# Kernel optimization log

Hardware: AMD Instinct MI355X
Metric: run time of the kernel (lower is better)

Reference implementation:

```python
import jax, jax.numpy as jnp
import numpy as np

B, T, S = 4, 16384, 256
V_DIM, L_DIM, E, H = 256, 768, 1024, 8
D = E // H  # head_dim = 128
SCALE = D ** -0.5
CLAMP = 50000.0


def setup_inputs() -> dict:
    key = jax.random.key(0)
    ks = jax.random.split(key, 8)
    w = lambda k, shp: jax.random.normal(k, shp, jnp.float32) * 0.03  # ~xavier scale
    return {
        'v': jax.random.normal(ks[0], (B, T, V_DIM), jnp.float32),
        'l': jax.random.normal(ks[1], (B, S, L_DIM), jnp.float32),
        'v_proj_w': w(ks[2], (V_DIM, E)), 'v_proj_b': jnp.zeros((E,), jnp.float32),
        'l_proj_w': w(ks[3], (L_DIM, E)), 'l_proj_b': jnp.zeros((E,), jnp.float32),
        'vv_w': w(ks[4], (V_DIM, E)), 'vv_b': jnp.zeros((E,), jnp.float32),
        'vl_w': w(ks[5], (L_DIM, E)), 'vl_b': jnp.zeros((E,), jnp.float32),
        'ov_w': w(ks[6], (E, V_DIM)), 'ov_b': jnp.zeros((V_DIM,), jnp.float32),
        'ol_w': w(ks[7], (E, L_DIM)), 'ol_b': jnp.zeros((L_DIM,), jnp.float32),
    }


def _heads(x):
    # [B, N, E] -> [B, H, N, D]
    b, n, _ = x.shape
    return x.reshape(b, n, H, D).transpose(0, 2, 1, 3)


def reference(v, l, v_proj_w, v_proj_b, l_proj_w, l_proj_b,
              vv_w, vv_b, vl_w, vl_b, ov_w, ov_b, ol_w, ol_b):
    b, t, _ = v.shape
    s = l.shape[1]
    q = _heads((v @ v_proj_w + v_proj_b) * SCALE)   # [B,H,T,D]
    k = _heads(l @ l_proj_w + l_proj_b)             # [B,H,S,D]
    val_v = _heads(v @ vv_w + vv_b)                 # [B,H,T,D]
    val_l = _heads(l @ vl_w + vl_b)                 # [B,H,S,D]

    attn = jnp.einsum('bhtd,bhsd->bhts', q, k)      # shared QK^T scores
    attn = jnp.clip(attn, -CLAMP, CLAMP)

    # column-direction softmax (over vision tokens) on the transpose
    attn_T = attn.transpose(0, 1, 3, 2)             # [B,H,S,T]
    attn_l = attn_T - jnp.max(attn_T, axis=-1, keepdims=True)
    attn_l = jnp.clip(attn_l, -CLAMP, CLAMP)
    attn_l = jax.nn.softmax(attn_l, axis=-1)

    # row-direction softmax (over text tokens)
    attn_v = jax.nn.softmax(attn, axis=-1)          # [B,H,T,S]

    out_v = jnp.einsum('bhts,bhsd->bhtd', attn_v, val_l)
    out_l = jnp.einsum('bhst,bhtd->bhsd', attn_l, val_v)
    out_v = out_v.transpose(0, 2, 1, 3).reshape(b, t, E)
    out_l = out_l.transpose(0, 2, 1, 3).reshape(b, s, E)
    return out_v @ ov_w + ov_b, out_l @ ol_w + ol_b
```

## Files before the change

### kernel.cpp

```cpp
#include <hip/hip_runtime.h>
#include <hip/hip_bf16.h>
#include <hip/hip_fp16.h>

#define DI __device__ __forceinline__

typedef short bf16x8 __attribute__((ext_vector_type(8)));
typedef float f32x4 __attribute__((ext_vector_type(4)));
using bf16 = __hip_bfloat16;

constexpr int Tn = 16384, Sn = 256, En = 1024;
constexpr float SCALEF = 0.08838834764831845f;
constexpr float CLAMPF = 50000.0f;

DI f32x4 mfma16(bf16x8 a, bf16x8 b, f32x4 c) {
  return __builtin_amdgcn_mfma_f32_16x16x32_bf16(a, b, c, 0, 0, 0);
}
DI unsigned short f2bu(float x) { bf16 h = __float2bfloat16(x); return *(unsigned short*)&h; }
DI unsigned int pack2(float lo, float hi) { return (unsigned)f2bu(lo) | ((unsigned)f2bu(hi) << 16); }
DI bf16x8 ldg8(const bf16* p) { return *(const bf16x8*)p; }
DI float clampf(float v) { return fminf(fmaxf(v, -CLAMPF), CLAMPF); }
DI unsigned int packh2(float a, float b) {
  __half2 h = __floats2half2_rn(a, b);
  return *(unsigned int*)&h;
}

__global__ void cast_weights(const float* __restrict__ w0, bf16* __restrict__ o0,
                             const float* __restrict__ w1, bf16* __restrict__ o1,
                             const float* __restrict__ w2, bf16* __restrict__ o2,
                             const float* __restrict__ w3, bf16* __restrict__ o3,
                             const float* __restrict__ w4, bf16* __restrict__ o4,
                             const float* __restrict__ w5, bf16* __restrict__ o5) {
  int id = blockIdx.x * 256 + threadIdx.x;
  switch (blockIdx.y) {
    case 0: if (id < 256*1024) { int k = id >> 10, n = id & 1023; o0[n*256 + k] = __float2bfloat16(w0[id]); } break;
    case 1: if (id < 256*1024) { int k = id >> 10, n = id & 1023; o1[n*256 + k] = __float2bfloat16(w1[id]); } break;
    case 2: if (id < 768*1024) { int k = id >> 10, n = id & 1023; o2[n*768 + k] = __float2bfloat16(w2[id]); } break;
    case 3: if (id < 768*1024) { int k = id >> 10, n = id & 1023; o3[n*768 + k] = __float2bfloat16(w3[id]); } break;
    case 4: if (id < 1024*256) { int k = id >> 8,  n = id & 255;  o4[n*1024 + k] = __float2bfloat16(w4[id]); } break;
    case 5: if (id < 1024*768) { int k = id / 768, n = id % 768;  o5[n*1024 + k] = __float2bfloat16(w5[id]); } break;
  }
}

template<int MODE>
__global__ __launch_bounds__(256) void gemm_kern(
    const void* __restrict__ A, const bf16* __restrict__ Bw0, const bf16* __restrict__ Bw1,
    const float* __restrict__ bias0, const float* __restrict__ bias1,
    void* __restrict__ out0, void* __restrict__ out1, int zbase)
{
  constexpr int K = (MODE == 0) ? 256 : (MODE == 1) ? 768 : 1024;
  const int z = blockIdx.z + zbase;
  const bf16* Bw = z ? Bw1 : Bw0;
  const float* bias = z ? bias1 : bias0;
  const int m0 = blockIdx.x * 128, n0 = blockIdx.y * 128;
  const int tid = threadIdx.x, lane = tid & 63;
  const int w = tid >> 6, wm = w >> 1, wn = w & 1;
  const int l15 = lane & 15, l4 = lane >> 4;

  __shared__ bf16 smem[128 * 136];
  bf16* As = smem;
  bf16* Bs = smem + 128 * 64;

  f32x4 acc[4][4];
  #pragma unroll
  for (int a = 0; a < 4; a++)
    #pragma unroll
    for (int c = 0; c < 4; c++) acc[a][c] = f32x4{0.f, 0.f, 0.f, 0.f};

  for (int k0 = 0; k0 < K; k0 += 64) {
    __syncthreads();
    #pragma unroll
    for (int it = 0; it < 4; it++) {
      int cid = it * 256 + tid;
      int row = cid >> 3, chk = cid & 7;
      uint4 va;
      if constexpr (MODE <= 1) {
        const float* ap = (const float*)A + (size_t)(m0 + row) * K + k0 + chk * 8;
        float4 f0 = *(const float4*)ap, f1 = *(const float4*)(ap + 4);
        va.x = pack2(f0.x, f0.y); va.y = pack2(f0.z, f0.w);
        va.z = pack2(f1.x, f1.y); va.w = pack2(f1.z, f1.w);
      } else {
        va = *reinterpret_cast<const uint4*>((const bf16*)A + (size_t)(m0 + row) * K + k0 + chk * 8);
      }
      *reinterpret_cast<uint4*>(As + row * 64 + ((chk ^ (row & 7)) * 8)) = va;
      uint4 vb = *reinterpret_cast<const uint4*>(Bw + (size_t)(n0 + row) * K + k0 + chk * 8);
      *reinterpret_cast<uint4*>(Bs + row * 64 + ((chk ^ (row & 7)) * 8)) = vb;
    }
    __syncthreads();
    #pragma unroll
    for (int ks = 0; ks < 2; ks++) {
      bf16x8 af[4], bfr[4];
      #pragma unroll
      for (int mf = 0; mf < 4; mf++) {
        int r = wm * 64 + mf * 16 + l15;
        af[mf] = *(const bf16x8*)(As + r * 64 + (((ks * 4 + l4) ^ (r & 7)) * 8));
      }
      #pragma unroll
      for (int nf = 0; nf < 4; nf++) {
        int r = wn * 64 + nf * 16 + l15;
        bfr[nf] = *(const bf16x8*)(Bs + r * 64 + (((ks * 4 + l4) ^ (r & 7)) * 8));
      }
      #pragma unroll
      for (int mf = 0; mf < 4; mf++)
        #pragma unroll
        for (int nf = 0; nf < 4; nf++)
          acc[mf][nf] = mfma16(af[mf], bfr[nf], acc[mf][nf]);
    }
  }
  __syncthreads();

  if constexpr (MODE <= 1) {
    #pragma unroll
    for (int nf = 0; nf < 4; nf++) {
      int nl = wn * 64 + nf * 16 + l15;
      float bv = bias[n0 + nl];
      #pragma unroll
      for (int mf = 0; mf < 4; mf++) {
        int ml = wm * 64 + mf * 16 + l4 * 4;
        #pragma unroll
        for (int i = 0; i < 4; i++) {
          float vv = acc[mf][nf][i] + bv;
          if (MODE == 0 && z == 0) vv *= SCALEF;
          smem[(ml + i) * 136 + nl] = __float2bfloat16(vv);
        }
      }
    }
    __syncthreads();
    constexpr int TT = (MODE == 0) ? Tn : Sn;
    const int h = n0 >> 7;
    const int r2 = tid >> 1, c0 = (tid & 1) * 64;
    if (z == 0) {
      int m = m0 + r2;
      int bq = (MODE == 0) ? 0 : (m >> 8);
      int t  = m & (TT - 1);
      bf16* out = (bf16*)out0;
      size_t base = ((size_t)(bq * 8 + h) * TT + t) * 128 + c0;
      #pragma unroll
      for (int j = 0; j < 32; j++) {
        unsigned int u = *(const unsigned int*)(smem + r2 * 136 + c0 + 2 * j);
        *(unsigned int*)(out + base + 2 * j) = u;
      }
    } else {
      int bq = (MODE == 0) ? 0 : (m0 >> 8);
      int t0 = m0 & (TT - 1);
      bf16* out = (bf16*)out1;
      size_t base = ((size_t)(bq * 8 + h) * 128 + r2) * TT + t0 + c0;
      #pragma unroll
      for (int j = 0; j < 32; j++) {
        unsigned short u0 = *(const unsigned short*)(smem + (c0 + 2 * j)     * 136 + r2);
        unsigned short u1 = *(const unsigned short*)(smem + (c0 + 2 * j + 1) * 136 + r2);
        *(unsigned int*)(out + base + 2 * j) = (unsigned)u0 | ((unsigned)u1 << 16);
      }
    }
  } else {
    constexpr int NOUT = (MODE == 2) ? 256 : 768;
    float* out = (float*)out0;
    #pragma unroll
    for (int nf = 0; nf < 4; nf++) {
      int n = n0 + wn * 64 + nf * 16 + l15;
      float bv = bias[n];
      #pragma unroll
      for (int mf = 0; mf < 4; mf++) {
        size_t mbase = (size_t)(m0 + wm * 64 + mf * 16 + l4 * 4) * NOUT + n;
        #pragma unroll
        for (int i = 0; i < 4; i++)
          out[mbase + (size_t)i * NOUT] = acc[mf][nf][i] + bv;
      }
    }
  }
}

template<int NCH, bool SLAB>
__global__ __launch_bounds__(512, 2) void attn_fused(
    const bf16* __restrict__ qh,
    const bf16* __restrict__ kh,
    const bf16* __restrict__ vallT,
    const bf16* __restrict__ valvT,
    bf16* __restrict__ ovh,
    void* __restrict__ col_dst,
    float* __restrict__ dsum_dst)
{
  constexpr int SPAN = Tn / NCH;
  constexpr int TILES = SPAN / 64;
  const int ch = blockIdx.x, h = blockIdx.y;
  const int tid = threadIdx.x, lane = tid & 63, w = tid >> 6;
  const int l15 = lane & 15, l4 = lane >> 4;
  const int sw = w * 32;
  const int e7 = l15 & 7;

  __shared__ bf16 Qb[2][64 * 128];
  __shared__ bf16 Vb[2][128 * 64];
  __shared__ bf16 Enat[64 * 264];
  __shared__ bf16 Etr[8][32 * 72];
  __shared__ float red[8][64];

  const bf16* qp  = qh    + (size_t)h * Tn * 128;
  const bf16* kp  = kh    + (size_t)h * Sn * 128;
  const bf16* vlp = vallT + (size_t)h * 128 * Sn;
  const bf16* vvp = valvT + (size_t)h * 128 * Tn;
  const int tb0 = ch * SPAN;

  bf16x8 bkr[4][2];
  #pragma unroll
  for (int ks = 0; ks < 4; ks++)
    #pragma unroll
    for (int si = 0; si < 2; si++)
      bkr[ks][si] = ldg8(kp + (size_t)(sw + si * 16 + l15) * 128 + ks * 32 + l4 * 8);
  bf16x8 bvr[8];
  #pragma unroll
  for (int ks2 = 0; ks2 < 8; ks2++)
    bvr[ks2] = ldg8(vlp + (size_t)(w * 16 + l15) * Sn + ks2 * 32 + l4 * 8);

  const int q_r0 = tid >> 4, q_c = tid & 15;
  const int q_r1 = q_r0 + 32;
  const int v_r0 = tid >> 3, v_c = tid & 7;
  const int v_r1 = v_r0 + 64;

  {
    uint4 q0 = *(const uint4*)(qp + (size_t)(tb0 + q_r0) * 128 + q_c * 8);
    uint4 q1 = *(const uint4*)(qp + (size_t)(tb0 + q_r1) * 128 + q_c * 8);
    uint4 v0 = *(const uint4*)(vvp + (size_t)v_r0 * Tn + tb0 + v_c * 8);
    uint4 v1 = *(const uint4*)(vvp + (size_t)v_r1 * Tn + tb0 + v_c * 8);
    *(uint4*)(&Qb[0][q_r0 * 128 + ((q_c ^ (q_r0 & 7)) * 8)]) = q0;
    *(uint4*)(&Qb[0][q_r1 * 128 + ((q_c ^ (q_r1 & 7)) * 8)]) = q1;
    *(uint4*)(&Vb[0][v_r0 * 64  + ((v_c ^ (v_r0 & 7)) * 8)]) = v0;
    *(uint4*)(&Vb[0][v_r1 * 64  + ((v_c ^ (v_r1 & 7)) * 8)]) = v1;
  }
  __syncthreads();

  f32x4 oc[8][2];
  #pragma unroll
  for (int a = 0; a < 8; a++)
    #pragma unroll
    for (int c = 0; c < 2; c++) oc[a][c] = f32x4{0.f, 0.f, 0.f, 0.f};
  float csum[2] = {0.f, 0.f};

  int cur = 0;
  for (int tt = 0; tt < TILES; tt++) {
    const int tb = tb0 + tt * 64;
    const bool hn = (tt + 1 < TILES);
    uint4 pfq0, pfq1, pfv0, pfv1;
    if (hn) {
      const int tbn = tb + 64;
      pfq0 = *(const uint4*)(qp + (size_t)(tbn + q_r0) * 128 + q_c * 8);
      pfq1 = *(const uint4*)(qp + (size_t)(tbn + q_r1) * 128 + q_c * 8);
      pfv0 = *(const uint4*)(vvp + (size_t)v_r0 * Tn + tbn + v_c * 8);
      pfv1 = *(const uint4*)(vvp + (size_t)v_r1 * Tn + tbn + v_c * 8);
    }
    f32x4 sacc[4][2];
    #pragma unroll
    for (int a = 0; a < 4; a++)
      #pragma unroll
      for (int c = 0; c < 2; c++) sacc[a][c] = f32x4{0.f, 0.f, 0.f, 0.f};
    #pragma unroll
    for (int ks = 0; ks < 4; ks++) {
      const int x = (ks * 4 + l4) ^ e7;
      bf16x8 aq[4];
      #pragma unroll
      for (int ti = 0; ti < 4; ti++)
        aq[ti] = *(const bf16x8*)(&Qb[cur][(ti * 16 + l15) * 128 + x * 8]);
      #pragma unroll
      for (int ti = 0; ti < 4; ti++)
        #pragma unroll
        for (int si = 0; si < 2; si++)
          sacc[ti][si] = mfma16(aq[ti], bkr[ks][si], sacc[ti][si]);
    }
    float rp[4][4];
    #pragma unroll
    for (int ti = 0; ti < 4; ti++)
      #pragma unroll
      for (int i = 0; i < 4; i++) rp[ti][i] = 0.f;
    #pragma unroll
    for (int ti = 0; ti < 4; ti++)
      #pragma unroll
      for (int si = 0; si < 2; si++) {
        float e0 = __expf(clampf(sacc[ti][si][0]));
        float e1 = __expf(clampf(sacc[ti][si][1]));
        float e2 = __expf(clampf(sacc[ti][si][2]));
        float e3 = __expf(clampf(sacc[ti][si][3]));
        csum[si] += (e0 + e1) + (e2 + e3);
        rp[ti][0] += e0; rp[ti][1] += e1; rp[ti][2] += e2; rp[ti][3] += e3;
        unsigned long long u = (unsigned long long)pack2(e0, e1) |
                               ((unsigned long long)pack2(e2, e3) << 32);
        *(unsigned long long*)(&Etr[w][(si * 16 + l15) * 72 + ti * 16 + l4 * 4]) = u;
        const int s = sw + si * 16 + l15;
        const int t0 = ti * 16 + l4 * 4;
        Enat[(t0 + 0) * 264 + s] = __float2bfloat16(e0);
        Enat[(t0 + 1) * 264 + s] = __float2bfloat16(e1);
        Enat[(t0 + 2) * 264 + s] = __float2bfloat16(e2);
        Enat[(t0 + 3) * 264 + s] = __float2bfloat16(e3);
      }
    #pragma unroll
    for (int ti = 0; ti < 4; ti++)
      #pragma unroll
      for (int i = 0; i < 4; i++) {
        float r = rp[ti][i];
        #pragma unroll
        for (int off = 1; off < 16; off <<= 1) r += __shfl_xor(r, off);
        if (l15 == 0) red[w][ti * 16 + l4 * 4 + i] = r;
      }
    __syncthreads();
    float rsm[4][4];
    #pragma unroll
    for (int ti = 0; ti < 4; ti++)
      #pragma unroll
      for (int i = 0; i < 4; i++) {
        const int tl = ti * 16 + l4 * 4 + i;
        float s = red[0][tl] + red[1][tl] + red[2][tl] + red[3][tl] +
                  red[4][tl] + red[5][tl] + red[6][tl] + red[7][tl];
        rsm[ti][i] = 1.0f / s;
      }
    f32x4 orr[4];
    #pragma unroll
    for (int a = 0; a < 4; a++) orr[a] = f32x4{0.f, 0.f, 0.f, 0.f};
    #pragma unroll
    for (int ks2 = 0; ks2 < 8; ks2++) {
      const int soff = ks2 * 32 + l4 * 8;
      #pragma unroll
      for (int ti = 0; ti < 4; ti++) {
        bf16x8 ap = *(const bf16x8*)(Enat + (ti * 16 + l15) * 264 + soff);
        orr[ti] = mfma16(ap, bvr[ks2], orr[ti]);
      }
    }
    #pragma unroll
    for (int ti = 0; ti < 4; ti++) {
      size_t base = (size_t)(tb + ti * 16 + l4 * 4) * En + h * 128 + w * 16 + l15;
      #pragma unroll
      for (int i = 0; i < 4; i++)
        ovh[base + (size_t)i * En] = __float2bfloat16(orr[ti][i] * rsm[ti][i]);
    }
    #pragma unroll
    for (int kst = 0; kst < 2; kst++) {
      bf16x8 bp[2];
      #pragma unroll
      for (int si = 0; si < 2; si++)
        bp[si] = *(const bf16x8*)(&Etr[w][(si * 16 + l15) * 72 + kst * 32 + l4 * 8]);
      const int x = (kst * 4 + l4) ^ e7;
      #pragma unroll
      for (int mf = 0; mf < 8; mf++) {
        bf16x8 av = *(const bf16x8*)(&Vb[cur][(mf * 16 + l15) * 64 + x * 8]);
        #pragma unroll
        for (int si = 0; si < 2; si++)
          oc[mf][si] = mfma16(av, bp[si], oc[mf][si]);
      }
    }
    if (hn) {
      *(uint4*)(&Qb[cur ^ 1][q_r0 * 128 + ((q_c ^ (q_r0 & 7)) * 8)]) = pfq0;
      *(uint4*)(&Qb[cur ^ 1][q_r1 * 128 + ((q_c ^ (q_r1 & 7)) * 8)]) = pfq1;
      *(uint4*)(&Vb[cur ^ 1][v_r0 * 64  + ((v_c ^ (v_r0 & 7)) * 8)]) = pfv0;
      *(uint4*)(&Vb[cur ^ 1][v_r1 * 64  + ((v_c ^ (v_r1 & 7)) * 8)]) = pfv1;
    }
    __syncthreads();
    cur ^= 1;
  }
  #pragma unroll
  for (int si = 0; si < 2; si++) {
    float c = csum[si];
    c += __shfl_xor(c, 16);
    c += __shfl_xor(c, 32);
    if (l4 == 0) {
      if constexpr (SLAB) dsum_dst[((size_t)(ch * 8 + h)) * 256 + sw + si * 16 + l15] = c;
      else atomicAdd(&dsum_dst[h * 256 + sw + si * 16 + l15], c);
    }
  }
  if constexpr (SLAB) {
    __half* slab = (__half*)col_dst + ((size_t)(ch * 8 + h) * 256) * 128;
    #pragma unroll
    for (int mf = 0; mf < 8; mf++)
      #pragma unroll
      for (int si = 0; si < 2; si++) {
        const int s = sw + si * 16 + l15;
        const int d = mf * 16 + l4 * 4;
        uint2 u;
        u.x = packh2(oc[mf][si][0], oc[mf][si][1]);
        u.y = packh2(oc[mf][si][2], oc[mf][si][3]);
        *(uint2*)(slab + (size_t)s * 128 + d) = u;
      }
  } else {
    float* olh = (float*)col_dst;
    #pragma unroll
    for (int mf = 0; mf < 8; mf++)
      #pragma unroll
      for (int si = 0; si < 2; si++) {
        const int s = sw + si * 16 + l15;
        const int d = mf * 16 + l4 * 4;
        float* dst = olh + (size_t)s * 1024 + h * 128 + d;
        #pragma unroll
        for (int i = 0; i < 4; i++) atomicAdd(dst + i, oc[mf][si][i]);
      }
  }
}

template<int NCH>
__global__ __launch_bounds__(256) void reduce_olh(
    const __half* __restrict__ slab, const float* __restrict__ csum_slab, bf16* __restrict__ olhb)
{
  int id = blockIdx.x * 256 + threadIdx.x;
  int s = id >> 8, hd4 = id & 255, h = hd4 >> 5, d4 = hd4 & 31;
  float a0 = 0.f, a1 = 0.f, a2 = 0.f, a3 = 0.f, dsv = 0.f;
  #pragma unroll 4
  for (int ch = 0; ch < NCH; ch++) {
    uint2 u = *(const uint2*)(slab + ((size_t)(ch * 8 + h) * 256 + s) * 128 + d4 * 4);
    __half2 x = *(__half2*)&u.x, y = *(__half2*)&u.y;
    a0 += __low2float(x); a1 += __high2float(x);
    a2 += __low2float(y); a3 += __high2float(y);
    dsv += csum_slab[((size_t)(ch * 8 + h)) * 256 + s];
  }
  float inv = 1.0f / dsv;
  unsigned long long u = (unsigned long long)pack2(a0 * inv, a1 * inv) |
                         ((unsigned long long)pack2(a2 * inv, a3 * inv) << 32);
  *reinterpret_cast<unsigned long long*>(olhb + (size_t)s * 1024 + h * 128 + d4 * 4) = u;
}

__global__ __launch_bounds__(256) void norm_olh(
    const float* __restrict__ olh, const float* __restrict__ dsum, bf16* __restrict__ olhb)
{
  int i = blockIdx.x * 256 + threadIdx.x;
  int s = i >> 8, c4 = i & 255;
  float inv = 1.0f / dsum[(c4 >> 5) * 256 + s];
  float4 x = reinterpret_cast<const float4*>(olh + (size_t)s * 1024)[c4];
  unsigned long long u = (unsigned long long)pack2(x.x * inv, x.y * inv) |
                         ((unsigned long long)pack2(x.z * inv, x.w * inv) << 32);
  *reinterpret_cast<unsigned long long*>(olhb + (size_t)s * 1024 + c4 * 4) = u;
}

extern "C" void kernel_launch(void* const* d_in, const int* in_sizes, int n_in,
                              void* d_out, int out_size, void* d_ws, size_t ws_size,
                              hipStream_t stream)
{
  (void)in_sizes; (void)n_in;
  const float* v        = (const float*)d_in[0];
  const float* l        = (const float*)d_in[1];
  const float* v_proj_w = (const float*)d_in[2];
  const float* v_proj_b = (const float*)d_in[3];
  const float* l_proj_w = (const float*)d_in[4];
  const float* l_proj_b = (const float*)d_in[5];
  const float* vv_w     = (const float*)d_in[6];
  const float* vv_b     = (const float*)d_in[7];
  const float* vl_w     = (const float*)d_in[8];
  const float* vl_b     = (const float*)d_in[9];
  const float* ov_w     = (const float*)d_in[10];
  const float* ov_b     = (const float*)d_in[11];
  const float* ol_w     = (const float*)d_in[12];
  const float* ol_b     = (const float*)d_in[13];

  char* ws = (char*)d_ws;
  size_t off = 0;
  auto alloc = [&](size_t bytes) -> char* {
    char* p = ws + off;
    off += (bytes + 255) & ~(size_t)255;
    return p;
  };

  bf16*  wqt   = (bf16*)alloc((size_t)1024 * 256 * 2);
  bf16*  wvvt  = (bf16*)alloc((size_t)1024 * 256 * 2);
  bf16*  wkt   = (bf16*)alloc((size_t)1024 * 768 * 2);
  bf16*  wvlt  = (bf16*)alloc((size_t)1024 * 768 * 2);
  bf16*  wovt  = (bf16*)alloc((size_t)256 * 1024 * 2);
  bf16*  wolt  = (bf16*)alloc((size_t)768 * 1024 * 2);
  bf16*  kh    = (bf16*)alloc((size_t)32 * 256 * 128 * 2);
  bf16*  vallT = (bf16*)alloc((size_t)32 * 128 * 256 * 2);
  float* olh   = (float*)alloc((size_t)1024 * 1024 * 4);
  bf16*  olhb  = (bf16*)alloc((size_t)1024 * 1024 * 2);
  float* dsum  = (float*)alloc((size_t)2048 * 4);
  bf16*  qh_b    = (bf16*)alloc((size_t)8 * 16384 * 128 * 2);
  bf16*  valvT_b = (bf16*)alloc((size_t)8 * 128 * 16384 * 2);
  bf16*  ovh_b   = (bf16*)alloc((size_t)16384 * 1024 * 2);
  const size_t off_base = off;

  const size_t slabh_b = (size_t)32 * 8 * 256 * 128 * 2;
  const size_t csum_b  = (size_t)32 * 8 * 256 * 4;
  int tier;
  if (off_base + slabh_b + csum_b <= ws_size) tier = 0;
  else if (off_base <= ws_size) tier = 2;
  else {
    hipMemsetAsync(d_out, 0xFF, (size_t)out_size * 4, stream);
    return;
  }
  __half* slabh     = (__half*)(ws + off_base);
  float*  csum_slab = (float*)(ws + off_base + slabh_b);

  if (tier == 2) hipMemsetAsync(olh, 0, (size_t)1024 * 1024 * 4, stream);

  cast_weights<<<dim3(3072, 6), 256, 0, stream>>>(v_proj_w, wqt, vv_w, wvvt,
                                                  l_proj_w, wkt, vl_w, wvlt, ov_w, wovt, ol_w, wolt);
  gemm_kern<1><<<dim3(8, 8, 2), 256, 0, stream>>>(l, wkt, wvlt, l_proj_b, vl_b, kh, vallT, 0);

  for (int b = 0; b < 4; b++) {
    const bf16*  kh_b    = kh    + (size_t)b * 8 * Sn * 128;
    const bf16*  vallT_b = vallT + (size_t)b * 8 * 128 * Sn;
    const float* v_b     = v + (size_t)b * 16384 * 256;
    gemm_kern<0><<<dim3(128, 8, 2), 256, 0, stream>>>(v_b, wqt, wvvt, v_proj_b, vv_b,
                                                      qh_b, valvT_b, 0);
    if (tier == 0) {
      attn_fused<32, true><<<dim3(32, 8), 512, 0, stream>>>(qh_b, kh_b, vallT_b, valvT_b,
                                                            ovh_b, slabh, csum_slab);
    } else {
      hipMemsetAsync(dsum, 0, (size_t)2048 * 4, stream);
      attn_fused<32, false><<<dim3(32, 8), 512, 0, stream>>>(qh_b, kh_b, vallT_b, valvT_b,
                                                             ovh_b, olh + (size_t)b * 256 * 1024, dsum);
    }
    gemm_kern<2><<<dim3(128, 2, 1), 256, 0, stream>>>(ovh_b, wovt, wovt, ov_b, ov_b,
                                                      (float*)d_out + (size_t)b * 16384 * 256, nullptr, 0);
    if (tier == 0) reduce_olh<32><<<256, 256, 0, stream>>>(slabh, csum_slab, olhb + (size_t)b * 256 * 1024);
    else           norm_olh<<<256, 256, 0, stream>>>(olh + (size_t)b * 256 * 1024, dsum,
                                                     olhb + (size_t)b * 256 * 1024);
  }

  gemm_kern<3><<<dim3(8, 6, 1), 256, 0, stream>>>(olhb, wolt, wolt, ol_b, ol_b,
                                                  (float*)d_out + 16777216, nullptr, 0);
}
```

Baseline: 676.4 us.

## Use direct global-to-LDS loads in GEMM and read Q straight from global in attention

The GEMM kernel now stages bf16 B (and A for bf16 mode) tiles with global_load_lds, writing swizzled rows directly into shared memory instead of going through registers. The attention kernel drops the Q shared-memory buffer and loads Q fragments directly from global memory per tile. It double-buffers Enat and the row-sum reduction array so one barrier per iteration is enough, and moves the V prefetch store to just after that barrier. This cuts LDS traffic and synchronization. The risks are exposed global latency on the Q loads and a changed hazard structure around the remaining single barrier.

Result: slower. 729.5 us (+7.9%).

```diff
diff --git a/kernel.cpp b/kernel.cpp
--- a/kernel.cpp
+++ b/kernel.cpp
@@ -7,6 +7,9 @@
 typedef short bf16x8 __attribute__((ext_vector_type(8)));
 typedef float f32x4 __attribute__((ext_vector_type(4)));
 using bf16 = __hip_bfloat16;
+
+typedef __attribute__((address_space(3))) void lds_void;
+typedef const __attribute__((address_space(1))) void glob_void;
 
 constexpr int Tn = 16384, Sn = 256, En = 1024;
 constexpr float SCALEF = 0.08838834764831845f;
@@ -22,6 +25,9 @@
 DI unsigned int packh2(float a, float b) {
   __half2 h = __floats2half2_rn(a, b);
   return *(unsigned int*)&h;
+}
+DI void gload16(const bf16* g, bf16* lds_base) {
+  __builtin_amdgcn_global_load_lds((glob_void*)g, (lds_void*)lds_base, 16, 0, 0);
 }
 
 __global__ void cast_weights(const float* __restrict__ w0, bf16* __restrict__ o0,
@@ -60,6 +66,9 @@
   bf16* As = smem;
   bf16* Bs = smem + 128 * 64;
 
+  const int wv = w, ln = lane;
+  const int lr = ln >> 3, lp = ln & 7;
+
   f32x4 acc[4][4];
   #pragma unroll
   for (int a = 0; a < 4; a++)
@@ -70,20 +79,30 @@
     __syncthreads();
     #pragma unroll
     for (int it = 0; it < 4; it++) {
-      int cid = it * 256 + tid;
-      int row = cid >> 3, chk = cid & 7;
-      uint4 va;
-      if constexpr (MODE <= 1) {
+      const int row = it * 32 + wv * 8 + lr;
+      const int gc = lp ^ (row & 7);
+      gload16(Bw + (size_t)(n0 + row) * K + k0 + gc * 8, Bs + (it * 32 + wv * 8) * 64);
+    }
+    if constexpr (MODE >= 2) {
+      #pragma unroll
+      for (int it = 0; it < 4; it++) {
+        const int row = it * 32 + wv * 8 + lr;
+        const int gc = lp ^ (row & 7);
+        gload16((const bf16*)A + (size_t)(m0 + row) * K + k0 + gc * 8,
+                As + (it * 32 + wv * 8) * 64);
+      }
+    } else {
+      #pragma unroll
+      for (int it = 0; it < 4; it++) {
+        int cid = it * 256 + tid;
+        int row = cid >> 3, chk = cid & 7;
         const float* ap = (const float*)A + (size_t)(m0 + row) * K + k0 + chk * 8;
         float4 f0 = *(const float4*)ap, f1 = *(const float4*)(ap + 4);
+        uint4 va;
         va.x = pack2(f0.x, f0.y); va.y = pack2(f0.z, f0.w);
         va.z = pack2(f1.x, f1.y); va.w = pack2(f1.z, f1.w);
-      } else {
-        va = *reinterpret_cast<const uint4*>((const bf16*)A + (size_t)(m0 + row) * K + k0 + chk * 8);
-      }
-      *reinterpret_cast<uint4*>(As + row * 64 + ((chk ^ (row & 7)) * 8)) = va;
-      uint4 vb = *reinterpret_cast<const uint4*>(Bw + (size_t)(n0 + row) * K + k0 + chk * 8);
-      *reinterpret_cast<uint4*>(Bs + row * 64 + ((chk ^ (row & 7)) * 8)) = vb;
+        *reinterpret_cast<uint4*>(As + row * 64 + ((chk ^ (row & 7)) * 8)) = va;
+      }
     }
     __syncthreads();
     #pragma unroll
@@ -187,11 +206,10 @@
   const int sw = w * 32;
   const int e7 = l15 & 7;
 
-  __shared__ bf16 Qb[2][64 * 128];
   __shared__ bf16 Vb[2][128 * 64];
-  __shared__ bf16 Enat[64 * 264];
+  __shared__ bf16 Enat[2][64 * 264];
   __shared__ bf16 Etr[8][32 * 72];
-  __shared__ float red[8][64];
+  __shared__ float red[2][8][64];
 
   const bf16* qp  = qh    + (size_t)h * Tn * 128;
   const bf16* kp  = kh    + (size_t)h * Sn * 128;
@@ -210,22 +228,15 @@
   for (int ks2 = 0; ks2 < 8; ks2++)
     bvr[ks2] = ldg8(vlp + (size_t)(w * 16 + l15) * Sn + ks2 * 32 + l4 * 8);
 
-  const int q_r0 = tid >> 4, q_c = tid & 15;
-  const int q_r1 = q_r0 + 32;
   const int v_r0 = tid >> 3, v_c = tid & 7;
   const int v_r1 = v_r0 + 64;
 
   {
-    uint4 q0 = *(const uint4*)(qp + (size_t)(tb0 + q_r0) * 128 + q_c * 8);
-    uint4 q1 = *(const uint4*)(qp + (size_t)(tb0 + q_r1) * 128 + q_c * 8);
     uint4 v0 = *(const uint4*)(vvp + (size_t)v_r0 * Tn + tb0 + v_c * 8);
     uint4 v1 = *(const uint4*)(vvp + (size_t)v_r1 * Tn + tb0 + v_c * 8);
-    *(uint4*)(&Qb[0][q_r0 * 128 + ((q_c ^ (q_r0 & 7)) * 8)]) = q0;
-    *(uint4*)(&Qb[0][q_r1 * 128 + ((q_c ^ (q_r1 & 7)) * 8)]) = q1;
-    *(uint4*)(&Vb[0][v_r0 * 64  + ((v_c ^ (v_r0 & 7)) * 8)]) = v0;
-    *(uint4*)(&Vb[0][v_r1 * 64  + ((v_c ^ (v_r1 & 7)) * 8)]) = v1;
-  }
-  __syncthreads();
+    *(uint4*)(&Vb[0][v_r0 * 64 + ((v_c ^ (v_r0 & 7)) * 8)]) = v0;
+    *(uint4*)(&Vb[0][v_r1 * 64 + ((v_c ^ (v_r1 & 7)) * 8)]) = v1;
+  }
 
   f32x4 oc[8][2];
   #pragma unroll
@@ -238,11 +249,9 @@
   for (int tt = 0; tt < TILES; tt++) {
     const int tb = tb0 + tt * 64;
     const bool hn = (tt + 1 < TILES);
-    uint4 pfq0, pfq1, pfv0, pfv1;
+    uint4 pfv0, pfv1;
     if (hn) {
       const int tbn = tb + 64;
-      pfq0 = *(const uint4*)(qp + (size_t)(tbn + q_r0) * 128 + q_c * 8);
-      pfq1 = *(const uint4*)(qp + (size_t)(tbn + q_r1) * 128 + q_c * 8);
       pfv0 = *(const uint4*)(vvp + (size_t)v_r0 * Tn + tbn + v_c * 8);
       pfv1 = *(const uint4*)(vvp + (size_t)v_r1 * Tn + tbn + v_c * 8);
     }
@@ -253,11 +262,11 @@
       for (int c = 0; c < 2; c++) sacc[a][c] = f32x4{0.f, 0.f, 0.f, 0.f};
     #pragma unroll
     for (int ks = 0; ks < 4; ks++) {
-      const int x = (ks * 4 + l4) ^ e7;
+      const int dof = ks * 32 + l4 * 8;
       bf16x8 aq[4];
       #pragma unroll
       for (int ti = 0; ti < 4; ti++)
-        aq[ti] = *(const bf16x8*)(&Qb[cur][(ti * 16 + l15) * 128 + x * 8]);
+        aq[ti] = ldg8(qp + (size_t)(tb + ti * 16 + l15) * 128 + dof);
       #pragma unroll
       for (int ti = 0; ti < 4; ti++)
         #pragma unroll
@@ -284,10 +293,10 @@
         *(unsigned long long*)(&Etr[w][(si * 16 + l15) * 72 + ti * 16 + l4 * 4]) = u;
         const int s = sw + si * 16 + l15;
         const int t0 = ti * 16 + l4 * 4;
-        Enat[(t0 + 0) * 264 + s] = __float2bfloat16(e0);
-        Enat[(t0 + 1) * 264 + s] = __float2bfloat16(e1);
-        Enat[(t0 + 2) * 264 + s] = __float2bfloat16(e2);
-        Enat[(t0 + 3) * 264 + s] = __float2bfloat16(e3);
+        Enat[cur][(t0 + 0) * 264 + s] = __float2bfloat16(e0);
+        Enat[cur][(t0 + 1) * 264 + s] = __float2bfloat16(e1);
+        Enat[cur][(t0 + 2) * 264 + s] = __float2bfloat16(e2);
+        Enat[cur][(t0 + 3) * 264 + s] = __float2bfloat16(e3);
       }
     #pragma unroll
     for (int ti = 0; ti < 4; ti++)
@@ -296,17 +305,21 @@
         float r = rp[ti][i];
         #pragma unroll
         for (int off = 1; off < 16; off <<= 1) r += __shfl_xor(r, off);
-        if (l15 == 0) red[w][ti * 16 + l4 * 4 + i] = r;
+        if (l15 == 0) red[cur][w][ti * 16 + l4 * 4 + i] = r;
       }
     __syncthreads();
+    if (hn) {
+      *(uint4*)(&Vb[cur ^ 1][v_r0 * 64 + ((v_c ^ (v_r0 & 7)) * 8)]) = pfv0;
+      *(uint4*)(&Vb[cur ^ 1][v_r1 * 64 + ((v_c ^ (v_r1 & 7)) * 8)]) = pfv1;
+    }
     float rsm[4][4];
     #pragma unroll
     for (int ti = 0; ti < 4; ti++)
       #pragma unroll
       for (int i = 0; i < 4; i++) {
         const int tl = ti * 16 + l4 * 4 + i;
-        float s = red[0][tl] + red[1][tl] + red[2][tl] + red[3][tl] +
-                  red[4][tl] + red[5][tl] + red[6][tl] + red[7][tl];
+        float s = red[cur][0][tl] + red[cur][1][tl] + red[cur][2][tl] + red[cur][3][tl] +
+                  red[cur][4][tl] + red[cur][5][tl] + red[cur][6][tl] + red[cur][7][tl];
         rsm[ti][i] = 1.0f / s;
       }
     f32x4 orr[4];
@@ -317,7 +330,7 @@
       const int soff = ks2 * 32 + l4 * 8;
       #pragma unroll
       for (int ti = 0; ti < 4; ti++) {
-        bf16x8 ap = *(const bf16x8*)(Enat + (ti * 16 + l15) * 264 + soff);
+        bf16x8 ap = *(const bf16x8*)(&Enat[cur][(ti * 16 + l15) * 264 + soff]);
         orr[ti] = mfma16(ap, bvr[ks2], orr[ti]);
       }
     }
@@ -343,13 +356,6 @@
           oc[mf][si] = mfma16(av, bp[si], oc[mf][si]);
       }
     }
-    if (hn) {
-      *(uint4*)(&Qb[cur ^ 1][q_r0 * 128 + ((q_c ^ (q_r0 & 7)) * 8)]) = pfq0;
-      *(uint4*)(&Qb[cur ^ 1][q_r1 * 128 + ((q_c ^ (q_r1 & 7)) * 8)]) = pfq1;
-      *(uint4*)(&Vb[cur ^ 1][v_r0 * 64  + ((v_c ^ (v_r0 & 7)) * 8)]) = pfv0;
-      *(uint4*)(&Vb[cur ^ 1][v_r1 * 64  + ((v_c ^ (v_r1 & 7)) * 8)]) = pfv1;
-    }
-    __syncthreads();
     cur ^= 1;
   }
   #pragma unroll
```

## Pre-cast activations to bf16 and stage GEMM tiles via direct global-to-LDS loads

Applied to the files above, without the earlier changes.

Adds a separate kernel that casts the fp32 inputs v and l to bf16 before the projection GEMMs. The GEMM tile loader can then use global_load_lds DMA for both operands, replacing register-staged loads, in-register conversion and LDS writes. The XOR swizzle moves from the LDS write address to the global source column. The trade is extra cast kernel launches and an extra round trip through memory for the activations, in exchange for cheaper tile staging in every GEMM mode.

Measured after the change: 646.0 us. 1.05x faster.

```diff
diff --git a/kernel.cpp b/kernel.cpp
--- a/kernel.cpp
+++ b/kernel.cpp
@@ -7,6 +7,9 @@
 typedef short bf16x8 __attribute__((ext_vector_type(8)));
 typedef float f32x4 __attribute__((ext_vector_type(4)));
 using bf16 = __hip_bfloat16;
+
+typedef __attribute__((address_space(3))) void lds_void;
+typedef const __attribute__((address_space(1))) void glob_void;
 
 constexpr int Tn = 16384, Sn = 256, En = 1024;
 constexpr float SCALEF = 0.08838834764831845f;
@@ -22,6 +25,18 @@
 DI unsigned int packh2(float a, float b) {
   __half2 h = __floats2half2_rn(a, b);
   return *(unsigned int*)&h;
+}
+DI void gload16(const bf16* g, bf16* lds_base) {
+  __builtin_amdgcn_global_load_lds((glob_void*)g, (lds_void*)lds_base, 16, 0, 0);
+}
+
+__global__ void cast_f32_bf16_v4(const float* __restrict__ in, bf16* __restrict__ out, int n4) {
+  int i = blockIdx.x * 256 + threadIdx.x;
+  if (i >= n4) return;
+  float4 f = reinterpret_cast<const float4*>(in)[i];
+  unsigned long long u = (unsigned long long)pack2(f.x, f.y) |
+                         ((unsigned long long)pack2(f.z, f.w) << 32);
+  *reinterpret_cast<unsigned long long*>(out + (size_t)i * 4) = u;
 }
 
 __global__ void cast_weights(const float* __restrict__ w0, bf16* __restrict__ o0,
@@ -43,7 +58,7 @@
 
 template<int MODE>
 __global__ __launch_bounds__(256) void gemm_kern(
-    const void* __restrict__ A, const bf16* __restrict__ Bw0, const bf16* __restrict__ Bw1,
+    const bf16* __restrict__ A, const bf16* __restrict__ Bw0, const bf16* __restrict__ Bw1,
     const float* __restrict__ bias0, const float* __restrict__ bias1,
     void* __restrict__ out0, void* __restrict__ out1, int zbase)
 {
@@ -60,6 +75,8 @@
   bf16* As = smem;
   bf16* Bs = smem + 128 * 64;
 
+  const int lr = lane >> 3, lp = lane & 7;
+
   f32x4 acc[4][4];
   #pragma unroll
   for (int a = 0; a < 4; a++)
@@ -70,20 +87,10 @@
     __syncthreads();
     #pragma unroll
     for (int it = 0; it < 4; it++) {
-      int cid = it * 256 + tid;
-      int row = cid >> 3, chk = cid & 7;
-      uint4 va;
-      if constexpr (MODE <= 1) {
-        const float* ap = (const float*)A + (size_t)(m0 + row) * K + k0 + chk * 8;
-        float4 f0 = *(const float4*)ap, f1 = *(const float4*)(ap + 4);
-        va.x = pack2(f0.x, f0.y); va.y = pack2(f0.z, f0.w);
-        va.z = pack2(f1.x, f1.y); va.w = pack2(f1.z, f1.w);
-      } else {
-        va = *reinterpret_cast<const uint4*>((const bf16*)A + (size_t)(m0 + row) * K + k0 + chk * 8);
-      }
-      *reinterpret_cast<uint4*>(As + row * 64 + ((chk ^ (row & 7)) * 8)) = va;
-      uint4 vb = *reinterpret_cast<const uint4*>(Bw + (size_t)(n0 + row) * K + k0 + chk * 8);
-      *reinterpret_cast<uint4*>(Bs + row * 64 + ((chk ^ (row & 7)) * 8)) = vb;
+      const int row = it * 32 + w * 8 + lr;
+      const int gc = lp ^ (row & 7);
+      gload16(Bw + (size_t)(n0 + row) * K + k0 + gc * 8, Bs + (it * 32 + w * 8) * 64);
+      gload16(A  + (size_t)(m0 + row) * K + k0 + gc * 8, As + (it * 32 + w * 8) * 64);
     }
     __syncthreads();
     #pragma unroll
@@ -457,11 +464,13 @@
   bf16*  wvlt  = (bf16*)alloc((size_t)1024 * 768 * 2);
   bf16*  wovt  = (bf16*)alloc((size_t)256 * 1024 * 2);
   bf16*  wolt  = (bf16*)alloc((size_t)768 * 1024 * 2);
+  bf16*  lb    = (bf16*)alloc((size_t)1024 * 768 * 2);
   bf16*  kh    = (bf16*)alloc((size_t)32 * 256 * 128 * 2);
   bf16*  vallT = (bf16*)alloc((size_t)32 * 128 * 256 * 2);
   float* olh   = (float*)alloc((size_t)1024 * 1024 * 4);
   bf16*  olhb  = (bf16*)alloc((size_t)1024 * 1024 * 2);
   float* dsum  = (float*)alloc((size_t)2048 * 4);
+  bf16*  vb_b    = (bf16*)alloc((size_t)16384 * 256 * 2);
   bf16*  qh_b    = (bf16*)alloc((size_t)8 * 16384 * 128 * 2);
   bf16*  valvT_b = (bf16*)alloc((size_t)8 * 128 * 16384 * 2);
   bf16*  ovh_b   = (bf16*)alloc((size_t)16384 * 1024 * 2);
@@ -483,13 +492,14 @@
 
   cast_weights<<<dim3(3072, 6), 256, 0, stream>>>(v_proj_w, wqt, vv_w, wvvt,
                                                   l_proj_w, wkt, vl_w, wvlt, ov_w, wovt, ol_w, wolt);
-  gemm_kern<1><<<dim3(8, 8, 2), 256, 0, stream>>>(l, wkt, wvlt, l_proj_b, vl_b, kh, vallT, 0);
+  cast_f32_bf16_v4<<<768, 256, 0, stream>>>(l, lb, 196608);
+  gemm_kern<1><<<dim3(8, 8, 2), 256, 0, stream>>>(lb, wkt, wvlt, l_proj_b, vl_b, kh, vallT, 0);
 
   for (int b = 0; b < 4; b++) {
     const bf16*  kh_b    = kh    + (size_t)b * 8 * Sn * 128;
     const bf16*  vallT_b = vallT + (size_t)b * 8 * 128 * Sn;
-    const float* v_b     = v + (size_t)b * 16384 * 256;
-    gemm_kern<0><<<dim3(128, 8, 2), 256, 0, stream>>>(v_b, wqt, wvvt, v_proj_b, vv_b,
+    cast_f32_bf16_v4<<<4096, 256, 0, stream>>>(v + (size_t)b * 16384 * 256, vb_b, 1048576);
+    gemm_kern<0><<<dim3(128, 8, 2), 256, 0, stream>>>(vb_b, wqt, wvvt, v_proj_b, vv_b,
                                                       qh_b, valvT_b, 0);
     if (tier == 0) {
       attn_fused<32, true><<<dim3(32, 8), 512, 0, stream>>>(qh_b, kh_b, vallT_b, valvT_b,
```
